# Kernel tuning notes

Measured on AMD Instinct MI355X. Metric: run time of the kernel, lower is better.

The kernel has to match this reference:

```python
import jax, jax.numpy as jnp
import numpy as np

H = 128; N = 64; B = 128; L = 3; F = 7; E = 64; LAT = 128
NEG = -1e9

def _ln(x, g, b, eps=1e-5):
    m = jnp.mean(x, axis=-1, keepdims=True)
    v = jnp.mean((x - m) ** 2, axis=-1, keepdims=True)
    return (x - m) / jnp.sqrt(v + eps) * g + b

def setup_inputs() -> dict:
    key = jax.random.key(0)
    ks = iter(jax.random.split(key, 64))
    def w(shape, s=0.05):
        return (jax.random.normal(next(ks), shape, dtype=jnp.float32) * s)
    inp = {}
    inp['battery_features'] = jax.random.normal(next(ks), (B, F), dtype=jnp.float32)
    inp['material_embeddings'] = jax.random.normal(next(ks), (B, N, E), dtype=jnp.float32)
    inp['node_mask'] = (jax.random.uniform(next(ks), (B, N)) > 0.2).astype(jnp.float32)
    # material encoder: Linear(E,H), LN, ReLU, Linear(H,H), LN, ReLU
    inp['enc_W1'] = w((E, H)); inp['enc_b1'] = jnp.zeros((H,))
    inp['enc_g1'] = jnp.ones((H,)); inp['enc_B1'] = jnp.zeros((H,))
    inp['enc_W2'] = w((H, H)); inp['enc_b2'] = jnp.zeros((H,))
    inp['enc_g2'] = jnp.ones((H,)); inp['enc_B2'] = jnp.zeros((H,))
    # per-layer GATv2 params (stacked over L layers)
    inp['Wq'] = w((L, H, H)); inp['bq'] = jnp.zeros((L, H))
    inp['Wk'] = w((L, H, H)); inp['bk'] = jnp.zeros((L, H))
    inp['Wv'] = w((L, H, H)); inp['bv'] = jnp.zeros((L, H))
    inp['We1'] = w((L, 2 * H, H)); inp['be1'] = jnp.zeros((L, H))
    inp['We2'] = w((L, H)); inp['be2'] = jnp.zeros((L,))
    inp['Wo'] = w((L, H, H)); inp['bo'] = jnp.zeros((L, H))
    inp['o_g'] = jnp.ones((L, H)); inp['o_B'] = jnp.zeros((L, H))
    # legacy decoder: Linear(F+H,H), LN, ReLU, Linear(H,LAT), LN, ReLU, Linear(LAT,F)
    inp['dW1'] = w((F + H, H)); inp['db1'] = jnp.zeros((H,))
    inp['dg1'] = jnp.ones((H,)); inp['dB1'] = jnp.zeros((H,))
    inp['dW2'] = w((H, LAT)); inp['db2'] = jnp.zeros((LAT,))
    inp['dg2'] = jnp.ones((LAT,)); inp['dB2'] = jnp.zeros((LAT,))
    inp['dW3'] = w((LAT, F)); inp['db3'] = jnp.zeros((F,))
    return inp

def reference(battery_features, material_embeddings, node_mask,
              enc_W1, enc_b1, enc_g1, enc_B1, enc_W2, enc_b2, enc_g2, enc_B2,
              Wq, bq, Wk, bk, Wv, bv, We1, be1, We2, be2, Wo, bo, o_g, o_B,
              dW1, db1, dg1, dB1, dW2, db2, dg2, dB2, dW3, db3):
    # material encoder (dropout=0 / eval)
    x = material_embeddings  # [B,N,E]
    h = jax.nn.relu(_ln(x @ enc_W1 + enc_b1, enc_g1, enc_B1))
    h = jax.nn.relu(_ln(h @ enc_W2 + enc_b2, enc_g2, enc_B2))
    x = h * node_mask[..., None]  # [B,N,H]
    mask2d = node_mask[:, :, None] * node_mask[:, None, :]  # [B,N,N]
    nlayers = Wq.shape[0]
    for l in range(nlayers):
        q = x @ Wq[l] + bq[l]
        k = x @ Wk[l] + bk[l]
        v = x @ Wv[l] + bv[l]
        # edge MLP on concat(q_i, k_j): split first linear, avoid concat materialization
        hq = q @ We1[l, :H]          # [B,N,H]
        hk = k @ We1[l, H:]          # [B,N,H]
        eh = jax.nn.relu(hq[:, :, None, :] + hk[:, None, :, :] + be1[l])  # [B,N,N,H]
        scores = jnp.einsum('bijh,h->bij', eh, We2[l]) + be2[l]
        scores = jnp.where(mask2d > 0, scores, NEG)
        attn = jax.nn.softmax(scores, axis=-1) * mask2d
        agg = jnp.einsum('bij,bjh->bih', attn, v)
        x = jax.nn.relu(_ln(agg @ Wo[l] + bo[l], o_g[l], o_B[l]))
        x = x * node_mask[..., None]
    # masked mean pooling
    denom = jnp.clip(jnp.sum(node_mask, axis=1, keepdims=True), 1.0, None)
    pooled = jnp.sum(x * node_mask[..., None], axis=1) / denom  # [B,H]
    d = jnp.concatenate([battery_features, pooled], axis=-1)
    z = jax.nn.relu(_ln(d @ dW1 + db1, dg1, dB1))
    z = jax.nn.relu(_ln(z @ dW2 + db2, dg2, dB2))
    return z @ dW3 + db3  # [B,F] predicted properties
```

## Files before the change

### kernel.cpp

```cpp
#include <hip/hip_runtime.h>


constexpr float EPS = 1e-5f;
constexpr float NEGI = -1e9f;

typedef __bf16 bf16x8 __attribute__((ext_vector_type(8)));
typedef float floatx4 __attribute__((ext_vector_type(4)));
typedef _Float16 h2 __attribute__((ext_vector_type(2)));
union U32H2 { unsigned int u; h2 h; };

__device__ __forceinline__ unsigned int pkh2(float a, float b) {
  U32H2 u; u.h[0] = (_Float16)a; u.h[1] = (_Float16)b; return u.u;
}
__device__ __forceinline__ float fdot2h(h2 a, h2 b, float c) {
#if __has_builtin(__builtin_amdgcn_fdot2)
  return __builtin_amdgcn_fdot2(a, b, c, false);
#else
  return c + (float)a[0] * (float)b[0] + (float)a[1] * (float)b[1];
#endif
}
__device__ __forceinline__ bf16x8 cvt8(const float* p) {
  float t[8];
  *(float4*)t = *(const float4*)p;
  *(float4*)(t + 4) = *(const float4*)(p + 4);
  bf16x8 r;
#pragma unroll
  for (int j = 0; j < 8; ++j) r[j] = (__bf16)t[j];
  return r;
}

__global__ __launch_bounds__(256) void prep_kernel(
    const float* __restrict__ Wq, const float* __restrict__ bq,
    const float* __restrict__ Wk, const float* __restrict__ bk,
    const float* __restrict__ bv, const float* __restrict__ We1,
    const float* __restrict__ be1,
    const float* __restrict__ eW1, const float* __restrict__ eW2,
    const float* __restrict__ Wv, const float* __restrict__ Wo,
    __bf16* __restrict__ w1pk, __bf16* __restrict__ w2pk,
    __bf16* __restrict__ wcatpk, __bf16* __restrict__ wopk,
    float* __restrict__ bcat) {
  int tid = threadIdx.x, blk = blockIdx.x;
  if (blk < 48) {
    __shared__ float sB[128 * 16];
    __shared__ float sF[128 * 17];
    int jb = blk >> 3, cc = blk & 7;
    int l = jb >> 1, w = jb & 1;
    const float* A = (w ? Wk : Wq) + l * 16384;
    const float* Bm = We1 + l * 32768 + w * 16384;
    int c0 = cc * 16;
    for (int idx = tid; idx < 2048; idx += 256) {
      int m = idx >> 4, c = idx & 15;
      sB[idx] = Bm[m * 128 + c0 + c];
    }
    __syncthreads();
    int r = tid >> 1, c8 = (tid & 1) * 8;
    float acc[8] = {};
    const float4* A4 = (const float4*)(A + r * 128);
#pragma unroll 8
    for (int k4 = 0; k4 < 32; ++k4) {
      float4 a = A4[k4];
      float av[4] = {a.x, a.y, a.z, a.w};
#pragma unroll
      for (int kk = 0; kk < 4; ++kk)
#pragma unroll
        for (int c = 0; c < 8; ++c)
          acc[c] = fmaf(av[kk], sB[(k4 * 4 + kk) * 16 + c8 + c], acc[c]);
    }
    for (int c = 0; c < 8; ++c) sF[r * 17 + c8 + c] = acc[c];
    __syncthreads();
    int kc = tid >> 6, ln = tid & 63;
    int k0 = kc * 32 + (ln >> 4) * 8, n = ln & 15;
    bf16x8 pk;
#pragma unroll
    for (int j = 0; j < 8; ++j) pk[j] = (__bf16)sF[(k0 + j) * 17 + n];
    int ntg = 8 + w * 8 + cc;
    *((bf16x8*)(wcatpk + l * 49152) + (ntg * 4 + kc) * 64 + ln) = pk;
  } else if (blk < 56) {
    int job = blk - 48;
    const float* src;
    __bf16* dst;
    int KCH = 4;
    if (job == 0) { src = eW1; dst = w1pk; KCH = 2; }
    else if (job == 1) { src = eW2; dst = w2pk; }
    else if (job < 5) { int l = job - 2; src = Wv + l * 16384; dst = wcatpk + l * 49152; }
    else { int l = job - 5; src = Wo + l * 16384; dst = wopk + l * 16384; }
    for (int s = tid; s < 8 * KCH * 64; s += 256) {
      int ln = s & 63, q = s >> 6;
      int kc = q % KCH, nt = q / KCH;
      int k0 = kc * 32 + (ln >> 4) * 8, n = nt * 16 + (ln & 15);
      bf16x8 pk;
#pragma unroll
      for (int j = 0; j < 8; ++j) pk[j] = (__bf16)src[(k0 + j) * 128 + n];
      *((bf16x8*)dst + (nt * KCH + kc) * 64 + ln) = pk;
    }
  } else {
    for (int idx = tid; idx < 3 * 384; idx += 256) {
      int l = idx / 384, c = idx % 384;
      float val;
      if (c < 128) {
        val = bv[l * 128 + c];
      } else if (c < 256) {
        int cc2 = c - 128;
        float s = 0.f;
        for (int k = 0; k < 128; ++k) s += bq[l * 128 + k] * We1[l * 32768 + k * 128 + cc2];
        val = s;
      } else {
        int cc2 = c - 256;
        float s = be1[l * 128 + cc2];
        for (int k = 0; k < 128; ++k) s += bk[l * 128 + k] * We1[l * 32768 + 16384 + k * 128 + cc2];
        val = s;
      }
      bcat[l * 384 + c] = val;
    }
  }
}

__device__ __forceinline__ void ln16(float* sT, __bf16* SX, const float* __restrict__ g,
                                     const float* __restrict__ be, float mreg,
                                     int i0, int tid, int mode) {
  int r = tid >> 4, c0 = tid & 15;
  const float* base = sT + r * 132;
  float s = 0.f, q = 0.f;
#pragma unroll
  for (int k = 0; k < 8; ++k) { float v = base[c0 + k * 16]; s += v; q += v * v; }
  s += __shfl_xor(s, 1); s += __shfl_xor(s, 2); s += __shfl_xor(s, 4); s += __shfl_xor(s, 8);
  q += __shfl_xor(q, 1); q += __shfl_xor(q, 2); q += __shfl_xor(q, 4); q += __shfl_xor(q, 8);
  float m = s * (1.f / 128.f);
  float rs = rsqrtf(fmaxf(q * (1.f / 128.f) - m * m, 0.f) + EPS);
  float mk = (mode >= 1) ? __shfl(mreg, i0 + r) : 1.f;
  int c8 = c0 * 8;
  float vals[8];
  *(float4*)vals = *(const float4*)(base + c8);
  *(float4*)(vals + 4) = *(const float4*)(base + c8 + 4);
#pragma unroll
  for (int k = 0; k < 8; ++k)
    vals[k] = fmaxf((vals[k] - m) * rs * g[c8 + k] + be[c8 + k], 0.f) * mk;
  if (mode < 2) {
    bf16x8 pk;
#pragma unroll
    for (int k = 0; k < 8; ++k) pk[k] = (__bf16)vals[k];
    ((bf16x8*)SX)[(c8 >> 5) * 64 + ((c8 >> 3) & 3) * 16 + r] = pk;
  } else {
    *(float4*)(sT + r * 132 + c8) = *(float4*)vals;
    *(float4*)(sT + r * 132 + c8 + 4) = *(float4*)(vals + 4);
  }
}

__device__ __forceinline__ void qkv_tail(
    const __bf16* SX, float* sTv,
    int b, int i0, const __bf16* __restrict__ wc, const float* __restrict__ bc,
    unsigned int* __restrict__ hqg_o, unsigned int* __restrict__ hkT_o,
    __bf16* __restrict__ vpk_o, int tid) {
  int lane = tid & 63, wv = tid >> 6, quad = lane >> 4, cl = lane & 15;
  bf16x8 ax[4];
#pragma unroll
  for (int kc = 0; kc < 4; ++kc) ax[kc] = ((const bf16x8*)SX)[kc * 64 + lane];
  floatx4 acc[6];
#pragma unroll
  for (int n = 0; n < 6; ++n) acc[n] = 0;
#pragma unroll
  for (int kc = 0; kc < 4; ++kc)
#pragma unroll
    for (int n = 0; n < 6; ++n) {
      bf16x8 bw = ((const bf16x8*)wc)[((wv + n * 4) * 4 + kc) * 64 + lane];
      if (n < 2)
        acc[n] = __builtin_amdgcn_mfma_f32_16x16x32_bf16(ax[kc], bw, acc[n], 0, 0, 0);
      else
        acc[n] = __builtin_amdgcn_mfma_f32_16x16x32_bf16(bw, ax[kc], acc[n], 0, 0, 0);
    }
#pragma unroll
  for (int n = 0; n < 6; ++n) {
    int g = wv + n * 4;
    if (n < 2) {
      int coll = g * 16 + cl;
      float bb = bc[coll];
#pragma unroll
      for (int r = 0; r < 4; ++r) sTv[(quad * 4 + r) * 132 + coll] = acc[n][r] + bb;
    } else if (n < 4) {
      int hb = (g - 8) * 16 + quad * 4;
      float4 bb4 = *(const float4*)(bc + 128 + hb);
      uint2 o;
      o.x = pkh2(acc[n][0] + bb4.x, acc[n][1] + bb4.y);
      o.y = pkh2(acc[n][2] + bb4.z, acc[n][3] + bb4.w);
      *(uint2*)(hqg_o + (b * 64 + i0 + cl) * 64 + (hb >> 1)) = o;
    } else {
      int hb = (g - 16) * 16 + quad * 4;
      float4 bb4 = *(const float4*)(bc + 256 + hb);
      hkT_o[b * 4096 + (hb >> 1) * 64 + i0 + cl] =
          pkh2(acc[n][0] + bb4.x, acc[n][1] + bb4.y);
      hkT_o[b * 4096 + ((hb >> 1) + 1) * 64 + i0 + cl] =
          pkh2(acc[n][2] + bb4.z, acc[n][3] + bb4.w);
    }
  }
  __syncthreads();
  {
    int nt = tid >> 5, dq = (tid >> 4) & 1, c2 = tid & 15;
    int kcv = i0 >> 5, qg = ((i0 & 31) >> 3) + dq;
    bf16x8 pk;
#pragma unroll
    for (int jj = 0; jj < 8; ++jj) pk[jj] = (__bf16)sTv[(dq * 8 + jj) * 132 + nt * 16 + c2];
    ((bf16x8*)vpk_o)[b * 1024 + (nt * 2 + kcv) * 64 + qg * 16 + c2] = pk;
  }
}

__global__ __launch_bounds__(256) void enc_qkv_kernel(
    const float* __restrict__ emb, const float* __restrict__ mask,
    const float* __restrict__ eb1, const float* __restrict__ eg1, const float* __restrict__ eB1,
    const float* __restrict__ eb2, const float* __restrict__ eg2, const float* __restrict__ eB2,
    const __bf16* __restrict__ w1pk, const __bf16* __restrict__ w2pk,
    const __bf16* __restrict__ wcat0, const float* __restrict__ bcat0,
    unsigned int* __restrict__ hqg, unsigned int* __restrict__ hkT,
    __bf16* __restrict__ vpk) {
  __shared__ __align__(16) __bf16 SX[2048];
  __shared__ __align__(16) float sTv[16 * 132];
  float* sT = sTv;
  int tid = threadIdx.x, blk = blockIdx.x;
  int lane = tid & 63, wv = tid >> 6, quad = lane >> 4, cl = lane & 15;
  int b = blk >> 2, i0 = (blk & 3) * 16;
  float mreg = mask[b * 64 + lane];

  {
    bf16x8 a1[2];
#pragma unroll
    for (int kc = 0; kc < 2; ++kc)
      a1[kc] = cvt8(emb + (b * 64 + i0 + cl) * 64 + kc * 32 + quad * 8);
    floatx4 acc[2];
    acc[0] = 0; acc[1] = 0;
#pragma unroll
    for (int kc = 0; kc < 2; ++kc)
#pragma unroll
      for (int n = 0; n < 2; ++n) {
        bf16x8 bw = ((const bf16x8*)w1pk)[((wv + n * 4) * 2 + kc) * 64 + lane];
        acc[n] = __builtin_amdgcn_mfma_f32_16x16x32_bf16(a1[kc], bw, acc[n], 0, 0, 0);
      }
#pragma unroll
    for (int n = 0; n < 2; ++n) {
      int col = (wv + n * 4) * 16 + cl;
      float bb = eb1[col];
#pragma unroll
      for (int r = 0; r < 4; ++r) sT[(quad * 4 + r) * 132 + col] = acc[n][r] + bb;
    }
  }
  __syncthreads();
  ln16(sT, SX, eg1, eB1, mreg, i0, tid, 0);
  __syncthreads();
  {
    bf16x8 a2[4];
#pragma unroll
    for (int kc = 0; kc < 4; ++kc) a2[kc] = ((const bf16x8*)SX)[kc * 64 + lane];
    floatx4 acc[2];
    acc[0] = 0; acc[1] = 0;
#pragma unroll
    for (int kc = 0; kc < 4; ++kc)
#pragma unroll
      for (int n = 0; n < 2; ++n) {
        bf16x8 bw = ((const bf16x8*)w2pk)[((wv + n * 4) * 4 + kc) * 64 + lane];
        acc[n] = __builtin_amdgcn_mfma_f32_16x16x32_bf16(a2[kc], bw, acc[n], 0, 0, 0);
      }
    __syncthreads();
#pragma unroll
    for (int n = 0; n < 2; ++n) {
      int col = (wv + n * 4) * 16 + cl;
      float bb = eb2[col];
#pragma unroll
      for (int r = 0; r < 4; ++r) sT[(quad * 4 + r) * 132 + col] = acc[n][r] + bb;
    }
  }
  __syncthreads();
  ln16(sT, SX, eg2, eB2, mreg, i0, tid, 1);
  __syncthreads();
  qkv_tail(SX, sTv, b, i0, wcat0, bcat0, hqg, hkT, vpk, tid);
}

template <bool LAST>
__global__ __launch_bounds__(256, 4) void layer_kernel(
    const unsigned int* __restrict__ hq_in, const unsigned int* __restrict__ hkT_in,
    const __bf16* __restrict__ vp_in, const float* __restrict__ mask,
    const float* __restrict__ We2l, const float* __restrict__ be2p,
    const __bf16* __restrict__ wopk_l, const float* __restrict__ bo_l,
    const float* __restrict__ og_l, const float* __restrict__ oB_l,
    const __bf16* __restrict__ wcat_n, const float* __restrict__ bcat_n,
    unsigned int* __restrict__ hq_out, unsigned int* __restrict__ hkT_out,
    __bf16* __restrict__ vpk_out, float* __restrict__ poolp) {
  __shared__ __align__(16) char SM[23040];
  unsigned int* hqS = (unsigned int*)(SM + 0);
  unsigned int* w2h = (unsigned int*)(SM + 4096);
  __bf16* pA  = (__bf16*)(SM + 4352);
  __bf16* pA2 = (__bf16*)(SM + 6400);
  __bf16* SX  = (__bf16*)(SM + 10496);
  float* sT   = (float*)(SM + 14592);
  float* sTv  = sT;
  int tid = threadIdx.x, blk = blockIdx.x;
  int lane = tid & 63, wv = tid >> 6, quad = lane >> 4, cl = lane & 15;
  int b = blk >> 2, i0 = (blk & 3) * 16;
  float mreg = mask[b * 64 + lane];

  {
    ((uint4*)hqS)[tid] = ((const uint4*)(hq_in + (b * 64 + i0) * 64))[tid];
    if (tid < 64) w2h[tid] = pkh2(We2l[2 * tid], We2l[2 * tid + 1]);
  }
  __syncthreads();

  {
    int j = lane;
    const unsigned int* hkg = hkT_in + b * 4096;
    float accs[4] = {0.f, 0.f, 0.f, 0.f};
    h2 hz = {(_Float16)0.0f, (_Float16)0.0f};
#pragma unroll 4
    for (int c4 = 0; c4 < 16; ++c4) {
      uint4 w2v = *(const uint4*)(w2h + c4 * 4);
      int hp0 = c4 * 4;
      uint4 hkv;
      hkv.x = hkg[(hp0 + 0) * 64 + j];
      hkv.y = hkg[(hp0 + 1) * 64 + j];
      hkv.z = hkg[(hp0 + 2) * 64 + j];
      hkv.w = hkg[(hp0 + 3) * 64 + j];
#pragma unroll
      for (int il = 0; il < 4; ++il) {
        uint4 hqv = *(const uint4*)(hqS + (wv * 4 + il) * 64 + hp0);
        U32H2 ha, hb, wc2;
        h2 s2;
        ha.u = hqv.x; hb.u = hkv.x; wc2.u = w2v.x;
        s2 = __builtin_elementwise_max(ha.h + hb.h, hz);
        accs[il] = fdot2h(s2, wc2.h, accs[il]);
        ha.u = hqv.y; hb.u = hkv.y; wc2.u = w2v.y;
        s2 = __builtin_elementwise_max(ha.h + hb.h, hz);
        accs[il] = fdot2h(s2, wc2.h, accs[il]);
        ha.u = hqv.z; hb.u = hkv.z; wc2.u = w2v.z;
        s2 = __builtin_elementwise_max(ha.h + hb.h, hz);
        accs[il] = fdot2h(s2, wc2.h, accs[il]);
        ha.u = hqv.w; hb.u = hkv.w; wc2.u = w2v.w;
        s2 = __builtin_elementwise_max(ha.h + hb.h, hz);
        accs[il] = fdot2h(s2, wc2.h, accs[il]);
      }
    }
    float be2v = be2p[0];
    float mj = mreg;
#pragma unroll
    for (int kk = 0; kk < 4; ++kk) {
      int il = wv * 4 + kk;
      float mi = __shfl(mreg, i0 + il);
      float m2 = mi * mj;
      float sc = (m2 > 0.f) ? accs[kk] + be2v : NEGI;
      float mx = sc;
#pragma unroll
      for (int off = 32; off >= 1; off >>= 1) mx = fmaxf(mx, __shfl_xor(mx, off));
      float p = __expf(sc - mx);
      float sm = p;
#pragma unroll
      for (int off = 32; off >= 1; off >>= 1) sm += __shfl_xor(sm, off);
      float a = p / sm * m2;
      pA[((j >> 5) * 64 + ((j >> 3) & 3) * 16 + il) * 8 + (j & 7)] = (__bf16)a;
    }
  }
  __syncthreads();

  {
    bf16x8 aat[2];
#pragma unroll
    for (int kc = 0; kc < 2; ++kc) aat[kc] = ((const bf16x8*)pA)[kc * 64 + lane];
    floatx4 acc[2];
    acc[0] = 0; acc[1] = 0;
#pragma unroll
    for (int kc = 0; kc < 2; ++kc)
#pragma unroll
      for (int n = 0; n < 2; ++n) {
        bf16x8 bw = ((const bf16x8*)vp_in)[b * 1024 + ((wv + n * 4) * 2 + kc) * 64 + lane];
        acc[n] = __builtin_amdgcn_mfma_f32_16x16x32_bf16(aat[kc], bw, acc[n], 0, 0, 0);
      }
#pragma unroll
    for (int n = 0; n < 2; ++n) {
      int hcol = (wv + n * 4) * 16 + cl;
#pragma unroll
      for (int r = 0; r < 4; ++r) {
        int i = quad * 4 + r;
        pA2[((hcol >> 5) * 64 + ((hcol >> 3) & 3) * 16 + i) * 8 + (hcol & 7)] =
            (__bf16)acc[n][r];
      }
    }
  }
  __syncthreads();

  {
    bf16x8 ag[4];
#pragma unroll
    for (int kc = 0; kc < 4; ++kc) ag[kc] = ((const bf16x8*)pA2)[kc * 64 + lane];
    floatx4 acc[2];
    acc[0] = 0; acc[1] = 0;
#pragma unroll
    for (int kc = 0; kc < 4; ++kc)
#pragma unroll
      for (int n = 0; n < 2; ++n) {
        bf16x8 bw = ((const bf16x8*)wopk_l)[((wv + n * 4) * 4 + kc) * 64 + lane];
        acc[n] = __builtin_amdgcn_mfma_f32_16x16x32_bf16(ag[kc], bw, acc[n], 0, 0, 0);
      }
#pragma unroll
    for (int n = 0; n < 2; ++n) {
      int col = (wv + n * 4) * 16 + cl;
      float bb = bo_l[col];
#pragma unroll
      for (int r = 0; r < 4; ++r) sT[(quad * 4 + r) * 132 + col] = acc[n][r] + bb;
    }
  }
  __syncthreads();
  ln16(sT, SX, og_l, oB_l, mreg, i0, tid, LAST ? 2 : 1);
  __syncthreads();
  if (!LAST) {
    qkv_tail(SX, sTv, b, i0, wcat_n, bcat_n, hq_out, hkT_out, vpk_out, tid);
  } else {
    if (tid < 128) {
      float s = 0.f;
#pragma unroll
      for (int r = 0; r < 16; ++r) s += sT[r * 132 + tid];
      poolp[blk * 128 + tid] = s;
    }
  }
}

__device__ __forceinline__ float ln128(float val, float g, float be, int t, float* red) {
  float s = val, q = val * val;
#pragma unroll
  for (int off = 32; off >= 1; off >>= 1) {
    s += __shfl_xor(s, off);
    q += __shfl_xor(q, off);
  }
  if ((t & 63) == 0) { red[(t >> 6) * 2] = s; red[(t >> 6) * 2 + 1] = q; }
  __syncthreads();
  float S = red[0] + red[2], Q = red[1] + red[3];
  __syncthreads();
  float m = S * (1.f / 128.f);
  float var = Q * (1.f / 128.f) - m * m;
  float r = rsqrtf(fmaxf(var, 0.f) + EPS);
  return (val - m) * r * g + be;
}

__global__ __launch_bounds__(128) void dec_kernel(
    const float* __restrict__ bfeat, const float* __restrict__ poolp,
    const float* __restrict__ mask,
    const float* __restrict__ dW1, const float* __restrict__ db1,
    const float* __restrict__ dg1, const float* __restrict__ dB1,
    const float* __restrict__ dW2, const float* __restrict__ db2,
    const float* __restrict__ dg2, const float* __restrict__ dB2,
    const float* __restrict__ dW3, const float* __restrict__ db3,
    float* __restrict__ out) {
  __shared__ float sd[136];
  __shared__ float sz[128];
  __shared__ float red[4];
  __shared__ float s_mk[64];
  int b = blockIdx.x, t = threadIdx.x;
  if (t < 64) s_mk[t] = mask[b * 64 + t];
  __syncthreads();
  float den = 0.f;
#pragma unroll
  for (int i = 0; i < 64; ++i) den += s_mk[i];
  den = fmaxf(den, 1.f);
  float pooled = poolp[(b * 4 + 0) * 128 + t] + poolp[(b * 4 + 1) * 128 + t] +
                 poolp[(b * 4 + 2) * 128 + t] + poolp[(b * 4 + 3) * 128 + t];
  if (t < 7) sd[t] = bfeat[b * 7 + t];
  sd[7 + t] = pooled / den;
  __syncthreads();

  float z = db1[t];
  for (int k = 0; k < 135; ++k) z = fmaf(sd[k], dW1[k * 128 + t], z);
  z = ln128(z, dg1[t], dB1[t], t, red);
  z = fmaxf(z, 0.f);
  sz[t] = z;
  __syncthreads();

  float z2 = db2[t];
  for (int k = 0; k < 128; ++k) z2 = fmaf(sz[k], dW2[k * 128 + t], z2);
  z2 = ln128(z2, dg2[t], dB2[t], t, red);
  z2 = fmaxf(z2, 0.f);
  sz[t] = z2;
  __syncthreads();

  if (t < 7) {
    float o = db3[t];
    for (int k = 0; k < 128; ++k) o = fmaf(sz[k], dW3[k * 7 + t], o);
    out[b * 7 + t] = o;
  }
}

extern "C" void kernel_launch(void* const* d_in, const int* in_sizes, int n_in,
                              void* d_out, int out_size, void* d_ws, size_t ws_size,
                              hipStream_t stream) {
  const float* bf   = (const float*)d_in[0];
  const float* emb  = (const float*)d_in[1];
  const float* mask = (const float*)d_in[2];
  const float* eW1 = (const float*)d_in[3];
  const float* eb1 = (const float*)d_in[4];
  const float* eg1 = (const float*)d_in[5];
  const float* eB1 = (const float*)d_in[6];
  const float* eW2 = (const float*)d_in[7];
  const float* eb2 = (const float*)d_in[8];
  const float* eg2 = (const float*)d_in[9];
  const float* eB2 = (const float*)d_in[10];
  const float* Wq = (const float*)d_in[11];
  const float* bq = (const float*)d_in[12];
  const float* Wk = (const float*)d_in[13];
  const float* bk = (const float*)d_in[14];
  const float* Wv = (const float*)d_in[15];
  const float* bv = (const float*)d_in[16];
  const float* We1 = (const float*)d_in[17];
  const float* be1 = (const float*)d_in[18];
  const float* We2 = (const float*)d_in[19];
  const float* be2 = (const float*)d_in[20];
  const float* Wo = (const float*)d_in[21];
  const float* bo = (const float*)d_in[22];
  const float* og = (const float*)d_in[23];
  const float* oB = (const float*)d_in[24];
  const float* dW1 = (const float*)d_in[25];
  const float* db1 = (const float*)d_in[26];
  const float* dg1 = (const float*)d_in[27];
  const float* dB1 = (const float*)d_in[28];
  const float* dW2 = (const float*)d_in[29];
  const float* db2 = (const float*)d_in[30];
  const float* dg2 = (const float*)d_in[31];
  const float* dB2 = (const float*)d_in[32];
  const float* dW3 = (const float*)d_in[33];
  const float* db3 = (const float*)d_in[34];
  float* out = (float*)d_out;

  char* ws = (char*)d_ws;
  float* bcat = (float*)(ws + 1024);
  __bf16* w1pk   = (__bf16*)(ws + 8192);
  __bf16* w2pk   = (__bf16*)(ws + 24576);
  __bf16* wcatpk = (__bf16*)(ws + 57344);
  __bf16* wopk   = (__bf16*)(ws + 352256);
  unsigned int* hqg = (unsigned int*)(ws + 524288);
  unsigned int* hkT = (unsigned int*)(ws + 4718592);
  __bf16* vpk = (__bf16*)(ws + 8912896);
  float* poolp = (float*)(ws + 13107200);

  prep_kernel<<<57, 256, 0, stream>>>(Wq, bq, Wk, bk, bv, We1, be1,
                                      eW1, eW2, Wv, Wo, w1pk, w2pk, wcatpk, wopk, bcat);
  enc_qkv_kernel<<<512, 256, 0, stream>>>(emb, mask, eb1, eg1, eB1, eb2, eg2, eB2,
                                          w1pk, w2pk, wcatpk, bcat, hqg, hkT, vpk);
  layer_kernel<false><<<512, 256, 0, stream>>>(
      hqg, hkT, vpk, mask, We2, be2, wopk, bo, og, oB,
      wcatpk + 49152, bcat + 384,
      hqg + 524288, hkT + 524288, vpk + 1048576, nullptr);
  layer_kernel<false><<<512, 256, 0, stream>>>(
      hqg + 524288, hkT + 524288, vpk + 1048576, mask, We2 + 128, be2 + 1,
      wopk + 16384, bo + 128, og + 128, oB + 128,
      wcatpk + 2 * 49152, bcat + 2 * 384,
      hqg, hkT, vpk, nullptr);
  layer_kernel<true><<<512, 256, 0, stream>>>(
      hqg, hkT, vpk, mask, We2 + 256, be2 + 2,
      wopk + 2 * 16384, bo + 256, og + 256, oB + 256,
      nullptr, nullptr, nullptr, nullptr, nullptr, poolp);
  dec_kernel<<<128, 128, 0, stream>>>(bf, poolp, mask, dW1, db1, dg1, dB1,
                                      dW2, db2, dg2, dB2, dW3, db3, out);
}
```

Baseline: 199.1 us.

## Prepack We2 once, read hq directly from global, split decoder K-loop

The fp16 packing of We2 moves into the prep kernel, so each layer block reads pre-packed weights from global memory. The attention score loop also reads hq straight from global memory instead of staging it in LDS, which removes a staging pass and a barrier and shrinks LDS use. The decoder kernel now runs 256 threads and splits each matvec's K loop across two halves combined through shared memory. The risk is higher global-load latency in the score loop without LDS reuse.

```diff
diff --git a/kernel.cpp b/kernel.cpp
--- a/kernel.cpp
+++ b/kernel.cpp
@@ -36,9 +36,10 @@
     const float* __restrict__ be1,
     const float* __restrict__ eW1, const float* __restrict__ eW2,
     const float* __restrict__ Wv, const float* __restrict__ Wo,
+    const float* __restrict__ We2,
     __bf16* __restrict__ w1pk, __bf16* __restrict__ w2pk,
     __bf16* __restrict__ wcatpk, __bf16* __restrict__ wopk,
-    float* __restrict__ bcat) {
+    float* __restrict__ bcat, unsigned int* __restrict__ w2hg) {
   int tid = threadIdx.x, blk = blockIdx.x;
   if (blk < 48) {
     __shared__ float sB[128 * 16];
@@ -112,6 +113,10 @@
       }
       bcat[l * 384 + c] = val;
     }
+    for (int idx = tid; idx < 192; idx += 256) {
+      int l = idx >> 6, c = idx & 63;
+      w2hg[l * 64 + c] = pkh2(We2[l * 128 + 2 * c], We2[l * 128 + 2 * c + 1]);
+    }
   }
 }
 
@@ -276,40 +281,33 @@
 __global__ __launch_bounds__(256, 4) void layer_kernel(
     const unsigned int* __restrict__ hq_in, const unsigned int* __restrict__ hkT_in,
     const __bf16* __restrict__ vp_in, const float* __restrict__ mask,
-    const float* __restrict__ We2l, const float* __restrict__ be2p,
+    const unsigned int* __restrict__ w2hl, const float* __restrict__ be2p,
     const __bf16* __restrict__ wopk_l, const float* __restrict__ bo_l,
     const float* __restrict__ og_l, const float* __restrict__ oB_l,
     const __bf16* __restrict__ wcat_n, const float* __restrict__ bcat_n,
     unsigned int* __restrict__ hq_out, unsigned int* __restrict__ hkT_out,
     __bf16* __restrict__ vpk_out, float* __restrict__ poolp) {
-  __shared__ __align__(16) char SM[23040];
-  unsigned int* hqS = (unsigned int*)(SM + 0);
-  unsigned int* w2h = (unsigned int*)(SM + 4096);
-  __bf16* pA  = (__bf16*)(SM + 4352);
-  __bf16* pA2 = (__bf16*)(SM + 6400);
-  __bf16* SX  = (__bf16*)(SM + 10496);
-  float* sT   = (float*)(SM + 14592);
-  float* sTv  = sT;
+  __shared__ __align__(16) __bf16 pA[1024];
+  __shared__ __align__(16) __bf16 pA2[2048];
+  __shared__ __align__(16) __bf16 SX[2048];
+  __shared__ __align__(16) float sTv[16 * 132];
+  float* sT = sTv;
   int tid = threadIdx.x, blk = blockIdx.x;
   int lane = tid & 63, wv = tid >> 6, quad = lane >> 4, cl = lane & 15;
   int b = blk >> 2, i0 = (blk & 3) * 16;
   float mreg = mask[b * 64 + lane];
 
   {
-    ((uint4*)hqS)[tid] = ((const uint4*)(hq_in + (b * 64 + i0) * 64))[tid];
-    if (tid < 64) w2h[tid] = pkh2(We2l[2 * tid], We2l[2 * tid + 1]);
-  }
-  __syncthreads();
-
-  {
     int j = lane;
     const unsigned int* hkg = hkT_in + b * 4096;
+    int wvu = __builtin_amdgcn_readfirstlane(wv);
+    const unsigned int* hqr = hq_in + (b * 64 + i0 + wvu * 4) * 64;
     float accs[4] = {0.f, 0.f, 0.f, 0.f};
     h2 hz = {(_Float16)0.0f, (_Float16)0.0f};
 #pragma unroll 4
     for (int c4 = 0; c4 < 16; ++c4) {
-      uint4 w2v = *(const uint4*)(w2h + c4 * 4);
       int hp0 = c4 * 4;
+      uint4 w2v = *(const uint4*)(w2hl + hp0);
       uint4 hkv;
       hkv.x = hkg[(hp0 + 0) * 64 + j];
       hkv.y = hkg[(hp0 + 1) * 64 + j];
@@ -317,7 +315,7 @@
       hkv.w = hkg[(hp0 + 3) * 64 + j];
 #pragma unroll
       for (int il = 0; il < 4; ++il) {
-        uint4 hqv = *(const uint4*)(hqS + (wv * 4 + il) * 64 + hp0);
+        uint4 hqv = *(const uint4*)(hqr + il * 64 + hp0);
         U32H2 ha, hb, wc2;
         h2 s2;
         ha.u = hqv.x; hb.u = hkv.x; wc2.u = w2v.x;
@@ -417,24 +415,7 @@
   }
 }
 
-__device__ __forceinline__ float ln128(float val, float g, float be, int t, float* red) {
-  float s = val, q = val * val;
-#pragma unroll
-  for (int off = 32; off >= 1; off >>= 1) {
-    s += __shfl_xor(s, off);
-    q += __shfl_xor(q, off);
-  }
-  if ((t & 63) == 0) { red[(t >> 6) * 2] = s; red[(t >> 6) * 2 + 1] = q; }
-  __syncthreads();
-  float S = red[0] + red[2], Q = red[1] + red[3];
-  __syncthreads();
-  float m = S * (1.f / 128.f);
-  float var = Q * (1.f / 128.f) - m * m;
-  float r = rsqrtf(fmaxf(var, 0.f) + EPS);
-  return (val - m) * r * g + be;
-}
-
-__global__ __launch_bounds__(128) void dec_kernel(
+__global__ __launch_bounds__(256) void dec_kernel(
     const float* __restrict__ bfeat, const float* __restrict__ poolp,
     const float* __restrict__ mask,
     const float* __restrict__ dW1, const float* __restrict__ db1,
@@ -443,41 +424,71 @@
     const float* __restrict__ dg2, const float* __restrict__ dB2,
     const float* __restrict__ dW3, const float* __restrict__ db3,
     float* __restrict__ out) {
-  __shared__ float sd[136];
-  __shared__ float sz[128];
+  __shared__ float sd[144];
+  __shared__ float part[256];
+  __shared__ float szz[128];
   __shared__ float red[4];
-  __shared__ float s_mk[64];
-  int b = blockIdx.x, t = threadIdx.x;
-  if (t < 64) s_mk[t] = mask[b * 64 + t];
-  __syncthreads();
-  float den = 0.f;
-#pragma unroll
-  for (int i = 0; i < 64; ++i) den += s_mk[i];
+  int b = blockIdx.x, tid = threadIdx.x;
+  int lane = tid & 63;
+  float mreg = mask[b * 64 + lane];
+  float den = mreg;
+#pragma unroll
+  for (int off = 32; off >= 1; off >>= 1) den += __shfl_xor(den, off);
   den = fmaxf(den, 1.f);
-  float pooled = poolp[(b * 4 + 0) * 128 + t] + poolp[(b * 4 + 1) * 128 + t] +
-                 poolp[(b * 4 + 2) * 128 + t] + poolp[(b * 4 + 3) * 128 + t];
-  if (t < 7) sd[t] = bfeat[b * 7 + t];
-  sd[7 + t] = pooled / den;
-  __syncthreads();
-
-  float z = db1[t];
-  for (int k = 0; k < 135; ++k) z = fmaf(sd[k], dW1[k * 128 + t], z);
-  z = ln128(z, dg1[t], dB1[t], t, red);
-  z = fmaxf(z, 0.f);
-  sz[t] = z;
-  __syncthreads();
-
-  float z2 = db2[t];
-  for (int k = 0; k < 128; ++k) z2 = fmaf(sz[k], dW2[k * 128 + t], z2);
-  z2 = ln128(z2, dg2[t], dB2[t], t, red);
-  z2 = fmaxf(z2, 0.f);
-  sz[t] = z2;
-  __syncthreads();
-
-  if (t < 7) {
-    float o = db3[t];
-    for (int k = 0; k < 128; ++k) o = fmaf(sz[k], dW3[k * 7 + t], o);
-    out[b * 7 + t] = o;
+  if (tid < 7) sd[tid] = bfeat[b * 7 + tid];
+  if (tid < 128) {
+    float pooled = poolp[(b * 4 + 0) * 128 + tid] + poolp[(b * 4 + 1) * 128 + tid] +
+                   poolp[(b * 4 + 2) * 128 + tid] + poolp[(b * 4 + 3) * 128 + tid];
+    sd[7 + tid] = pooled / den;
+  }
+  __syncthreads();
+  int t = tid & 127, g2 = tid >> 7;
+  {
+    float zp = 0.f;
+    for (int k = g2; k < 135; k += 2) zp = fmaf(sd[k], dW1[k * 128 + t], zp);
+    part[g2 * 128 + t] = zp;
+  }
+  __syncthreads();
+  {
+    float z = db1[t] + part[t] + part[128 + t];
+    float s = z, q = z * z;
+#pragma unroll
+    for (int off = 32; off >= 1; off >>= 1) { s += __shfl_xor(s, off); q += __shfl_xor(q, off); }
+    if (tid < 128 && lane == 0) { red[(tid >> 6) * 2] = s; red[(tid >> 6) * 2 + 1] = q; }
+    __syncthreads();
+    float S = red[0] + red[2], Q = red[1] + red[3];
+    float m = S * (1.f / 128.f);
+    float rs = rsqrtf(fmaxf(Q * (1.f / 128.f) - m * m, 0.f) + EPS);
+    z = fmaxf((z - m) * rs * dg1[t] + dB1[t], 0.f);
+    __syncthreads();
+    if (tid < 128) szz[t] = z;
+  }
+  __syncthreads();
+  {
+    float zp = 0.f;
+    for (int k = g2; k < 128; k += 2) zp = fmaf(szz[k], dW2[k * 128 + t], zp);
+    part[g2 * 128 + t] = zp;
+  }
+  __syncthreads();
+  {
+    float y = db2[t] + part[t] + part[128 + t];
+    float s = y, q = y * y;
+#pragma unroll
+    for (int off = 32; off >= 1; off >>= 1) { s += __shfl_xor(s, off); q += __shfl_xor(q, off); }
+    if (tid < 128 && lane == 0) { red[(tid >> 6) * 2] = s; red[(tid >> 6) * 2 + 1] = q; }
+    __syncthreads();
+    float S = red[0] + red[2], Q = red[1] + red[3];
+    float m = S * (1.f / 128.f);
+    float rs = rsqrtf(fmaxf(Q * (1.f / 128.f) - m * m, 0.f) + EPS);
+    y = fmaxf((y - m) * rs * dg2[t] + dB2[t], 0.f);
+    __syncthreads();
+    if (tid < 128) szz[t] = y;
+  }
+  __syncthreads();
+  if (tid < 7) {
+    float o = db3[tid];
+    for (int k = 0; k < 128; ++k) o = fmaf(szz[k], dW3[k * 7 + tid], o);
+    out[b * 7 + tid] = o;
   }
 }
 
@@ -523,6 +534,7 @@
 
   char* ws = (char*)d_ws;
   float* bcat = (float*)(ws + 1024);
+  unsigned int* w2hg = (unsigned int*)(ws + 6144);
   __bf16* w1pk   = (__bf16*)(ws + 8192);
   __bf16* w2pk   = (__bf16*)(ws + 24576);
   __bf16* wcatpk = (__bf16*)(ws + 57344);
@@ -533,22 +545,23 @@
   float* poolp = (float*)(ws + 13107200);
 
   prep_kernel<<<57, 256, 0, stream>>>(Wq, bq, Wk, bk, bv, We1, be1,
-                                      eW1, eW2, Wv, Wo, w1pk, w2pk, wcatpk, wopk, bcat);
+                                      eW1, eW2, Wv, Wo, We2,
+                                      w1pk, w2pk, wcatpk, wopk, bcat, w2hg);
   enc_qkv_kernel<<<512, 256, 0, stream>>>(emb, mask, eb1, eg1, eB1, eb2, eg2, eB2,
                                           w1pk, w2pk, wcatpk, bcat, hqg, hkT, vpk);
   layer_kernel<false><<<512, 256, 0, stream>>>(
-      hqg, hkT, vpk, mask, We2, be2, wopk, bo, og, oB,
+      hqg, hkT, vpk, mask, w2hg, be2, wopk, bo, og, oB,
       wcatpk + 49152, bcat + 384,
       hqg + 524288, hkT + 524288, vpk + 1048576, nullptr);
   layer_kernel<false><<<512, 256, 0, stream>>>(
-      hqg + 524288, hkT + 524288, vpk + 1048576, mask, We2 + 128, be2 + 1,
+      hqg + 524288, hkT + 524288, vpk + 1048576, mask, w2hg + 64, be2 + 1,
       wopk + 16384, bo + 128, og + 128, oB + 128,
       wcatpk + 2 * 49152, bcat + 2 * 384,
       hqg, hkT, vpk, nullptr);
   layer_kernel<true><<<512, 256, 0, stream>>>(
-      hqg, hkT, vpk, mask, We2 + 256, be2 + 2,
+      hqg, hkT, vpk, mask, w2hg + 128, be2 + 2,
       wopk + 2 * 16384, bo + 256, og + 256, oB + 256,
       nullptr, nullptr, nullptr, nullptr, nullptr, poolp);
-  dec_kernel<<<128, 128, 0, stream>>>(bf, poolp, mask, dW1, db1, dg1, dB1,
+  dec_kernel<<<128, 256, 0, stream>>>(bf, poolp, mask, dW1, db1, dg1, dB1,
                                       dW2, db2, dg2, dB2, dW3, db3, out);
 }
```

Result: slower. 222.0 us (+11.5%).
